# Kernel optimization log

Hardware: AMD Instinct MI355X
Metric: run time of the kernel (lower is better)

Reference implementation:

```python
import jax, jax.numpy as jnp
import numpy as np

BN_EPS = 1e-5

def bn(x, gamma, beta):
    # x: [N, C]; BatchNorm2d over (batch, spatial) == node axis here (training-mode batch stats)
    mu = x.mean(axis=0, keepdims=True)
    var = x.var(axis=0, keepdims=True)
    return (x - mu) * jax.lax.rsqrt(var + BN_EPS) * gamma + beta

def octree_conv(x, neigh, W):
    # x: [N, Cin]; neigh: [N, K] with values in [0, N], N == empty neighbor
    # W: [K, Cin, Cout]. Sparse octree conv = neighbor gather + contraction.
    xp = jnp.concatenate([x, jnp.zeros((1, x.shape[1]), x.dtype)], axis=0)  # zero row for empties
    g = xp[neigh]                                  # [N, K, Cin]
    return jnp.einsum('nkc,kcd->nd', g, W)         # [N, Cout]

def setup_inputs() -> dict:
    key = jax.random.key(0)
    ks = jax.random.split(key, 8)
    N, Cin, Cout, Cb, K = 60000, 256, 512, 128, 27
    s = 0.05
    return {
        'x': jax.random.normal(ks[0], (1, Cin, N, 1), jnp.float32),
        'neigh': jax.random.randint(ks[1], (N, K), 0, N + 1),
        'W1a': jax.random.normal(ks[2], (Cb, Cin), jnp.float32) * s,
        'g1a': jnp.ones((Cb,), jnp.float32), 'b1a': jnp.zeros((Cb,), jnp.float32),
        'W3': jax.random.normal(ks[3], (K, Cb, Cb), jnp.float32) * s,
        'g3': jnp.ones((Cb,), jnp.float32), 'b3': jnp.zeros((Cb,), jnp.float32),
        'W1b': jax.random.normal(ks[4], (Cout, Cb), jnp.float32) * s,
        'g1b': jnp.ones((Cout,), jnp.float32), 'b1b': jnp.zeros((Cout,), jnp.float32),
        'Wc': jax.random.normal(ks[5], (Cout, Cin), jnp.float32) * s,
        'gc': jnp.ones((Cout,), jnp.float32), 'bc': jnp.zeros((Cout,), jnp.float32),
    }

def reference(x, neigh, W1a, g1a, b1a, W3, g3, b3, W1b, g1b, b1b, Wc, gc, bc):
    h = jnp.squeeze(x, axis=(0, 3)).T                         # [N, Cin]
    c1 = jax.nn.relu(bn(h @ W1a.T, g1a, b1a))                 # 1x1 conv + BN + ReLU -> [N, Cb]
    c2 = jax.nn.relu(bn(octree_conv(c1, neigh, W3), g3, b3))  # sparse 3x3 octree conv + BN + ReLU
    c3 = bn(c2 @ W1b.T, g1b, b1b)                             # 1x1 conv + BN -> [N, Cout]
    sc = bn(h @ Wc.T, gc, bc)                                 # shortcut 1x1 conv + BN (Cin != Cout)
    out = jax.nn.relu(c3 + sc)
    return out.T[None, :, :, None]                            # [1, Cout, N, 1]
```

## Files before the change

kernel.cpp:

```cpp
#include <hip/hip_runtime.h>


typedef __bf16 bf16x8 __attribute__((ext_vector_type(8)));
typedef float f32x4 __attribute__((ext_vector_type(4)));
typedef unsigned short u16x8 __attribute__((ext_vector_type(8)));
typedef unsigned short u16x4 __attribute__((ext_vector_type(4)));

__device__ __forceinline__ unsigned short f2bfu(float f) {
  union { float f; unsigned u; } v; v.f = f;
  unsigned r = v.u + 0x7fffu + ((v.u >> 16) & 1u);
  return (unsigned short)(r >> 16);
}
__device__ __forceinline__ float bfu2f(unsigned short s) {
  union { unsigned u; float f; } v; v.u = ((unsigned)s) << 16;
  return v.f;
}

__device__ __forceinline__ void gload_lds16(const unsigned short* g, unsigned short* l) {
  __builtin_amdgcn_global_load_lds(
      (const __attribute__((address_space(1))) unsigned int*)(unsigned long long)g,
      (__attribute__((address_space(3))) unsigned int*)(unsigned int)(unsigned long long)l,
      16, 0, 0);
}

__device__ __forceinline__ int xcd_swz(int bid, int nwg) {
  int q = nwg >> 3, r = nwg & 7;
  int xcd = bid & 7, idx = bid >> 3;
  int base = xcd < r ? xcd * (q + 1) : r * (q + 1) + (xcd - r) * q;
  return base + idx;
}

__global__ __launch_bounds__(256) void prep_transpose(
    const float* __restrict__ x, unsigned short* __restrict__ h,
    const float* __restrict__ W1a, const float* __restrict__ W3,
    const float* __restrict__ W1b, const float* __restrict__ Wc,
    unsigned short* __restrict__ w1a, unsigned short* __restrict__ w3t,
    unsigned short* __restrict__ w1b, unsigned short* __restrict__ wc,
    int M, int MT) {
  __shared__ float tile[64][65];
  int t = threadIdx.x;
  if (blockIdx.x < 432) {
    int i = blockIdx.x * 256 + t;
    for (; i < 442368; i += 432 * 256) {
      if (i < 32768)  w1a[i] = f2bfu(W1a[i]);
      if (i < 65536)  w1b[i] = f2bfu(W1b[i]);
      if (i < 131072) wc[i]  = f2bfu(Wc[i]);
      int k = i >> 14, rr = i & 16383;
      int d = rr >> 7, c = rr & 127;
      w3t[i] = f2bfu(W3[(k << 14) + (c << 7) + d]);
    }
    return;
  }
  int bid = blockIdx.x - 432;
  int n0 = (bid % MT) * 64, c0 = (bid / MT) * 64;
  int nl = t & 63;
#pragma unroll
  for (int i = 0; i < 16; ++i) {
    int cl = i * 4 + (t >> 6);
    int n = n0 + nl;
    tile[cl][nl] = (n < M) ? x[(size_t)(c0 + cl) * M + n] : 0.f;
  }
  __syncthreads();
  int cl = t & 63;
#pragma unroll
  for (int i = 0; i < 16; ++i) {
    int nl2 = i * 4 + (t >> 6);
    int n = n0 + nl2;
    h[(size_t)n * 256 + c0 + cl] = f2bfu(tile[cl][nl2]);
  }
}

__global__ __launch_bounds__(512, 4) void gemm128(
    const unsigned short* __restrict__ A, const unsigned short* __restrict__ W,
    unsigned short* __restrict__ C, float* __restrict__ partials,
    int M, int Kd, int Nc, int ncol) {
  __shared__ unsigned short sA[2][128 * 64];
  __shared__ unsigned short sB[2][128 * 64];
  __shared__ float sStat[8][2][128];
  int t = threadIdx.x, wave = t >> 6, lane = t & 63;
  int flat = xcd_swz(blockIdx.x, gridDim.x);
  int n0 = (flat % ncol) * 128;
  int rowt = flat / ncol;
  int m0 = rowt * 128;
  int wr = wave >> 1, wcc = wave & 1;
  int l4 = lane >> 4, lc = lane & 15, lc7 = lc & 7;
  int lrow = lane >> 3, lch = lane & 7;
  f32x4 acc[2][4] = {};
  const int np = Kd >> 6;

  auto STAGE = [&](int p, int buf) {
    int k0 = p << 6;
#pragma unroll
    for (int i = 0; i < 2; ++i) {
      int row = wave * 16 + i * 8 + lrow;
      int sc = lch ^ (row & 7);
      gload_lds16(A + (size_t)(m0 + row) * Kd + k0 + sc * 8, &sA[buf][(wave * 16 + i * 8) * 64]);
    }
#pragma unroll
    for (int i = 0; i < 2; ++i) {
      int row = wave * 16 + i * 8 + lrow;
      int sc = lch ^ (row & 7);
      gload_lds16(W + (size_t)(n0 + row) * Kd + k0 + sc * 8, &sB[buf][(wave * 16 + i * 8) * 64]);
    }
  };
  auto COMPUTE = [&](int buf) {
#pragma unroll
    for (int kk = 0; kk < 2; ++kk) {
      bf16x8 af[2], bfr[4];
#pragma unroll
      for (int mi = 0; mi < 2; ++mi) {
        int row = wr * 32 + mi * 16 + lc;
        int chunk = (kk * 4 + l4) ^ lc7;
        af[mi] = __builtin_bit_cast(bf16x8, *(const u16x8*)(&sA[buf][row * 64 + chunk * 8]));
      }
#pragma unroll
      for (int ni = 0; ni < 4; ++ni) {
        int row = wcc * 64 + ni * 16 + lc;
        int chunk = (kk * 4 + l4) ^ lc7;
        bfr[ni] = __builtin_bit_cast(bf16x8, *(const u16x8*)(&sB[buf][row * 64 + chunk * 8]));
      }
      __builtin_amdgcn_s_setprio(1);
#pragma unroll
      for (int mi = 0; mi < 2; ++mi)
#pragma unroll
        for (int ni = 0; ni < 4; ++ni)
          acc[mi][ni] = __builtin_amdgcn_mfma_f32_16x16x32_bf16(af[mi], bfr[ni], acc[mi][ni], 0, 0, 0);
      __builtin_amdgcn_s_setprio(0);
    }
  };

  STAGE(0, 0);
  for (int p = 0; p < np; ++p) {
    int cur = p & 1;
    if (p < np - 1) {
      STAGE(p + 1, cur ^ 1);
      asm volatile("s_waitcnt vmcnt(4)" ::: "memory");
    } else {
      asm volatile("s_waitcnt vmcnt(0)" ::: "memory");
    }
    __builtin_amdgcn_sched_barrier(0);
    __builtin_amdgcn_s_barrier();
    __builtin_amdgcn_sched_barrier(0);
    COMPUTE(cur);
    __builtin_amdgcn_sched_barrier(0);
    __builtin_amdgcn_s_barrier();
  }

#pragma unroll
  for (int ni = 0; ni < 4; ++ni) {
    float s = 0.f, q = 0.f;
    int col = wcc * 64 + ni * 16 + lc;
#pragma unroll
    for (int mi = 0; mi < 2; ++mi)
#pragma unroll
      for (int j = 0; j < 4; ++j) {
        int n = m0 + wr * 32 + mi * 16 + l4 * 4 + j;
        unsigned short u = f2bfu(acc[mi][ni][j]);
        if (n < M) C[(size_t)n * Nc + n0 + col] = u;
        float v = bfu2f(u);
        s += v; q += v * v;
      }
    s += __shfl_xor(s, 16); s += __shfl_xor(s, 32);
    q += __shfl_xor(q, 16); q += __shfl_xor(q, 32);
    if (lane < 16) {
      sStat[wave][0][col] = s;
      sStat[wave][1][col] = q;
    }
  }
  __syncthreads();
  if (t < 128) {
    int wcs = t >> 6;
    float s = 0.f, q = 0.f;
#pragma unroll
    for (int g = 0; g < 4; ++g) {
      s += sStat[g * 2 + wcs][0][t];
      q += sStat[g * 2 + wcs][1][t];
    }
    partials[(size_t)rowt * (2 * Nc) + n0 + t] = s;
    partials[(size_t)rowt * (2 * Nc) + Nc + n0 + t] = q;
  }
}

__global__ __launch_bounds__(512, 4) void octree_sc(
    const unsigned short* __restrict__ c1, const int* __restrict__ neigh,
    const unsigned short* __restrict__ w3t, unsigned short* __restrict__ c2p,
    float* __restrict__ part12,
    const unsigned short* __restrict__ h, const unsigned short* __restrict__ wc,
    unsigned short* __restrict__ scp, float* __restrict__ partsc,
    int M, int MTO) {
  __shared__ unsigned short sA[2][128 * 64];
  __shared__ unsigned short sB[2][128 * 64];
  __shared__ union {
    unsigned short nidx[128 * 27];
    float stat[8][2][128];
  } u;
  int t = threadIdx.x, wave = t >> 6, lane = t & 63;
  int wr = wave >> 1, wcc = wave & 1;
  int l4 = lane >> 4, lc = lane & 15, lc7 = lc & 7;
  int lrow = lane >> 3, lch = lane & 7;
  f32x4 acc[2][4] = {};

  if (blockIdx.x < (unsigned)MTO) {
    int rowt = blockIdx.x;
    int m0 = rowt * 128;
    for (int i = t; i < 128 * 27; i += 512) {
      int row = i / 27;
      u.nidx[i] = (unsigned short)((m0 + row < M) ? neigh[(size_t)m0 * 27 + i] : M);
    }
    __syncthreads();

    auto STAGE = [&](int p, int buf) {
      int half = (p >= 27) ? 1 : 0;
      int k = p - half * 27;
      int c0 = half << 6;
#pragma unroll
      for (int i = 0; i < 2; ++i) {
        int row = wave * 16 + i * 8 + lrow;
        int nr = u.nidx[row * 27 + k];
        int sc = lch ^ (row & 7);
        gload_lds16(c1 + ((size_t)nr << 7) + c0 + sc * 8, &sA[buf][(wave * 16 + i * 8) * 64]);
      }
      const unsigned short* wk = w3t + ((size_t)k << 14);
#pragma unroll
      for (int i = 0; i < 2; ++i) {
        int row = wave * 16 + i * 8 + lrow;
        int sc = lch ^ (row & 7);
        gload_lds16(wk + ((size_t)row << 7) + c0 + sc * 8, &sB[buf][(wave * 16 + i * 8) * 64]);
      }
    };
    auto COMPUTE = [&](int buf) {
#pragma unroll
      for (int kk = 0; kk < 2; ++kk) {
        bf16x8 af[2], bfr[4];
#pragma unroll
        for (int mi = 0; mi < 2; ++mi) {
          int row = wr * 32 + mi * 16 + lc;
          int chunk = (kk * 4 + l4) ^ lc7;
          af[mi] = __builtin_bit_cast(bf16x8, *(const u16x8*)(&sA[buf][row * 64 + chunk * 8]));
        }
#pragma unroll
        for (int ni = 0; ni < 4; ++ni) {
          int row = wcc * 64 + ni * 16 + lc;
          int chunk = (kk * 4 + l4) ^ lc7;
          bfr[ni] = __builtin_bit_cast(bf16x8, *(const u16x8*)(&sB[buf][row * 64 + chunk * 8]));
        }
        __builtin_amdgcn_s_setprio(1);
#pragma unroll
        for (int mi = 0; mi < 2; ++mi)
#pragma unroll
          for (int ni = 0; ni < 4; ++ni)
            acc[mi][ni] = __builtin_amdgcn_mfma_f32_16x16x32_bf16(af[mi], bfr[ni], acc[mi][ni], 0, 0, 0);
        __builtin_amdgcn_s_setprio(0);
      }
    };

    STAGE(0, 0);
    for (int p = 0; p < 54; ++p) {
      int cur = p & 1;
      if (p < 53) {
        STAGE(p + 1, cur ^ 1);
        asm volatile("s_waitcnt vmcnt(4)" ::: "memory");
      } else {
        asm volatile("s_waitcnt vmcnt(0)" ::: "memory");
      }
      __builtin_amdgcn_sched_barrier(0);
      __builtin_amdgcn_s_barrier();
      __builtin_amdgcn_sched_barrier(0);
      COMPUTE(cur);
      __builtin_amdgcn_sched_barrier(0);
      __builtin_amdgcn_s_barrier();
    }

#pragma unroll
    for (int ni = 0; ni < 4; ++ni) {
      float s = 0.f, q = 0.f;
      int col = wcc * 64 + ni * 16 + lc;
#pragma unroll
      for (int mi = 0; mi < 2; ++mi)
#pragma unroll
        for (int j = 0; j < 4; ++j) {
          int n = m0 + wr * 32 + mi * 16 + l4 * 4 + j;
          unsigned short uo = f2bfu(acc[mi][ni][j]);
          if (n < M) c2p[(size_t)n * 128 + col] = uo;
          float v = bfu2f(uo);
          s += v; q += v * v;
        }
      s += __shfl_xor(s, 16); s += __shfl_xor(s, 32);
      q += __shfl_xor(q, 16); q += __shfl_xor(q, 32);
      if (lane < 16) {
        u.stat[wave][0][col] = s;
        u.stat[wave][1][col] = q;
      }
    }
    __syncthreads();
    if (t < 128) {
      int wcs = t >> 6;
      float s = 0.f, q = 0.f;
#pragma unroll
      for (int g = 0; g < 4; ++g) {
        s += u.stat[g * 2 + wcs][0][t];
        q += u.stat[g * 2 + wcs][1][t];
      }
      part12[(size_t)rowt * 256 + t] = s;
      part12[(size_t)rowt * 256 + 128 + t] = q;
    }
    return;
  }

  {
    int flat = xcd_swz(blockIdx.x - MTO, gridDim.x - MTO);
    int n0 = (flat & 3) * 128;
    int rowt = flat >> 2;
    int m0 = rowt * 128;

    auto STAGE = [&](int p, int buf) {
      int k0 = p << 6;
#pragma unroll
      for (int i = 0; i < 2; ++i) {
        int row = wave * 16 + i * 8 + lrow;
        int sc = lch ^ (row & 7);
        gload_lds16(h + (size_t)(m0 + row) * 256 + k0 + sc * 8, &sA[buf][(wave * 16 + i * 8) * 64]);
      }
#pragma unroll
      for (int i = 0; i < 2; ++i) {
        int row = wave * 16 + i * 8 + lrow;
        int sc = lch ^ (row & 7);
        gload_lds16(wc + (size_t)(n0 + row) * 256 + k0 + sc * 8, &sB[buf][(wave * 16 + i * 8) * 64]);
      }
    };
    auto COMPUTE = [&](int buf) {
#pragma unroll
      for (int kk = 0; kk < 2; ++kk) {
        bf16x8 af[2], bfr[4];
#pragma unroll
        for (int mi = 0; mi < 2; ++mi) {
          int row = wr * 32 + mi * 16 + lc;
          int chunk = (kk * 4 + l4) ^ lc7;
          af[mi] = __builtin_bit_cast(bf16x8, *(const u16x8*)(&sA[buf][row * 64 + chunk * 8]));
        }
#pragma unroll
        for (int ni = 0; ni < 4; ++ni) {
          int row = wcc * 64 + ni * 16 + lc;
          int chunk = (kk * 4 + l4) ^ lc7;
          bfr[ni] = __builtin_bit_cast(bf16x8, *(const u16x8*)(&sB[buf][row * 64 + chunk * 8]));
        }
        __builtin_amdgcn_s_setprio(1);
#pragma unroll
        for (int mi = 0; mi < 2; ++mi)
#pragma unroll
          for (int ni = 0; ni < 4; ++ni)
            acc[mi][ni] = __builtin_amdgcn_mfma_f32_16x16x32_bf16(af[mi], bfr[ni], acc[mi][ni], 0, 0, 0);
        __builtin_amdgcn_s_setprio(0);
      }
    };

    STAGE(0, 0);
    for (int p = 0; p < 4; ++p) {
      int cur = p & 1;
      if (p < 3) {
        STAGE(p + 1, cur ^ 1);
        asm volatile("s_waitcnt vmcnt(4)" ::: "memory");
      } else {
        asm volatile("s_waitcnt vmcnt(0)" ::: "memory");
      }
      __builtin_amdgcn_sched_barrier(0);
      __builtin_amdgcn_s_barrier();
      __builtin_amdgcn_sched_barrier(0);
      COMPUTE(cur);
      __builtin_amdgcn_sched_barrier(0);
      __builtin_amdgcn_s_barrier();
    }

#pragma unroll
    for (int ni = 0; ni < 4; ++ni) {
      float s = 0.f, q = 0.f;
      int col = wcc * 64 + ni * 16 + lc;
#pragma unroll
      for (int mi = 0; mi < 2; ++mi)
#pragma unroll
        for (int j = 0; j < 4; ++j) {
          int n = m0 + wr * 32 + mi * 16 + l4 * 4 + j;
          unsigned short uo = f2bfu(acc[mi][ni][j]);
          if (n < M) scp[(size_t)n * 512 + n0 + col] = uo;
          float v = bfu2f(uo);
          s += v; q += v * v;
        }
      s += __shfl_xor(s, 16); s += __shfl_xor(s, 32);
      q += __shfl_xor(q, 16); q += __shfl_xor(q, 32);
      if (lane < 16) {
        u.stat[wave][0][col] = s;
        u.stat[wave][1][col] = q;
      }
    }
    __syncthreads();
    if (t < 128) {
      int wcs = t >> 6;
      float s = 0.f, q = 0.f;
#pragma unroll
      for (int g = 0; g < 4; ++g) {
        s += u.stat[g * 2 + wcs][0][t];
        q += u.stat[g * 2 + wcs][1][t];
      }
      partsc[(size_t)rowt * 1024 + n0 + t] = s;
      partsc[(size_t)rowt * 1024 + 512 + n0 + t] = q;
    }
  }
}

__global__ __launch_bounds__(256) void bn_finalize(
    const float* __restrict__ partials, int nb, int C, int M,
    const float* __restrict__ g, const float* __restrict__ bt,
    float* __restrict__ ss) {
  int c = blockIdx.x;
  int t = threadIdx.x;
  float s = 0.f, s2 = 0.f;
  for (int b = t; b < nb; b += 256) {
    s += partials[(size_t)b * 2 * C + c];
    s2 += partials[(size_t)b * 2 * C + C + c];
  }
#pragma unroll
  for (int off = 32; off >= 1; off >>= 1) {
    s += __shfl_xor(s, off);
    s2 += __shfl_xor(s2, off);
  }
  __shared__ float sh[4][2];
  int wave = t >> 6, lane = t & 63;
  if (lane == 0) { sh[wave][0] = s; sh[wave][1] = s2; }
  __syncthreads();
  if (t == 0) {
    s = sh[0][0] + sh[1][0] + sh[2][0] + sh[3][0];
    s2 = sh[0][1] + sh[1][1] + sh[2][1] + sh[3][1];
    float mean = s / (float)M;
    float var = s2 / (float)M - mean * mean;
    float sc = g[c] * rsqrtf(var + 1e-5f);
    ss[c] = sc;
    ss[C + c] = bt[c] - mean * sc;
  }
}

__global__ __launch_bounds__(256) void bn_finalize_dual(
    const float* __restrict__ part12, const float* __restrict__ partsc,
    int nb, int M,
    const float* __restrict__ g3, const float* __restrict__ b3,
    const float* __restrict__ gc, const float* __restrict__ bc,
    float* __restrict__ ss2, float* __restrict__ sssc) {
  const float* partials; const float* g; const float* bt; float* ss;
  int c, C;
  if (blockIdx.x < 128) {
    partials = part12; g = g3; bt = b3; ss = ss2; c = blockIdx.x; C = 128;
  } else {
    partials = partsc; g = gc; bt = bc; ss = sssc; c = blockIdx.x - 128; C = 512;
  }
  int t = threadIdx.x;
  float s = 0.f, s2 = 0.f;
  for (int b = t; b < nb; b += 256) {
    s += partials[(size_t)b * 2 * C + c];
    s2 += partials[(size_t)b * 2 * C + C + c];
  }
#pragma unroll
  for (int off = 32; off >= 1; off >>= 1) {
    s += __shfl_xor(s, off);
    s2 += __shfl_xor(s2, off);
  }
  __shared__ float sh[4][2];
  int wave = t >> 6, lane = t & 63;
  if (lane == 0) { sh[wave][0] = s; sh[wave][1] = s2; }
  __syncthreads();
  if (t == 0) {
    s = sh[0][0] + sh[1][0] + sh[2][0] + sh[3][0];
    s2 = sh[0][1] + sh[1][1] + sh[2][1] + sh[3][1];
    float mean = s / (float)M;
    float var = s2 / (float)M - mean * mean;
    float sc = g[c] * rsqrtf(var + 1e-5f);
    ss[c] = sc;
    ss[C + c] = bt[c] - mean * sc;
  }
}

__global__ __launch_bounds__(256) void bnrelu(
    const unsigned short* __restrict__ P, const float* __restrict__ ss,
    unsigned short* __restrict__ Aout, int total, int total2, int Cmask) {
  int i = (blockIdx.x * 256 + threadIdx.x) * 8;
  if (i >= total2) return;
  u16x8 o = {0, 0, 0, 0, 0, 0, 0, 0};
  if (i < total) {
    u16x8 v = *(const u16x8*)(P + i);
    int c0 = i & Cmask;
    int C = Cmask + 1;
#pragma unroll
    for (int j = 0; j < 8; ++j) {
      float f = bfu2f(v[j]) * ss[c0 + j] + ss[C + c0 + j];
      o[j] = f2bfu(fmaxf(f, 0.f));
    }
  }
  *(u16x8*)(Aout + i) = o;
}

__global__ __launch_bounds__(256) void final_out(
    const unsigned short* __restrict__ c3p, const unsigned short* __restrict__ scp,
    const float* __restrict__ ss3, const float* __restrict__ sssc,
    float* __restrict__ out, int M) {
  __shared__ float tile[64][129];
  int n0 = blockIdx.x * 64, c0 = blockIdx.y * 128;
  int t = threadIdx.x;
  int rowg = t >> 5, cg = (t & 31) * 4;
#pragma unroll
  for (int ps = 0; ps < 8; ++ps) {
    int nl = ps * 8 + rowg;
    int n = n0 + nl;
    float v0 = 0.f, v1 = 0.f, v2 = 0.f, v3 = 0.f;
    if (n < M) {
      u16x4 a = *(const u16x4*)(c3p + (size_t)n * 512 + c0 + cg);
      u16x4 b = *(const u16x4*)(scp + (size_t)n * 512 + c0 + cg);
      int c = c0 + cg;
      v0 = fmaxf(bfu2f(a[0]) * ss3[c + 0] + ss3[512 + c + 0] + bfu2f(b[0]) * sssc[c + 0] + sssc[512 + c + 0], 0.f);
      v1 = fmaxf(bfu2f(a[1]) * ss3[c + 1] + ss3[512 + c + 1] + bfu2f(b[1]) * sssc[c + 1] + sssc[512 + c + 1], 0.f);
      v2 = fmaxf(bfu2f(a[2]) * ss3[c + 2] + ss3[512 + c + 2] + bfu2f(b[2]) * sssc[c + 2] + sssc[512 + c + 2], 0.f);
      v3 = fmaxf(bfu2f(a[3]) * ss3[c + 3] + ss3[512 + c + 3] + bfu2f(b[3]) * sssc[c + 3] + sssc[512 + c + 3], 0.f);
    }
    tile[nl][cg + 0] = v0;
    tile[nl][cg + 1] = v1;
    tile[nl][cg + 2] = v2;
    tile[nl][cg + 3] = v3;
  }
  __syncthreads();
  int nl = t & 63, cq = t >> 6;
  int n = n0 + nl;
  if (n < M) {
#pragma unroll
    for (int i = 0; i < 32; ++i) {
      int cl = i * 4 + cq;
      out[(size_t)(c0 + cl) * M + n] = tile[nl][cl];
    }
  }
}

extern "C" void kernel_launch(void* const* d_in, const int* in_sizes, int n_in,
                              void* d_out, int out_size, void* d_ws, size_t ws_size,
                              hipStream_t stream) {
  const float* x   = (const float*)d_in[0];
  const int* neigh = (const int*)d_in[1];
  const float* W1a = (const float*)d_in[2];
  const float* g1a = (const float*)d_in[3];
  const float* b1a = (const float*)d_in[4];
  const float* W3  = (const float*)d_in[5];
  const float* g3  = (const float*)d_in[6];
  const float* b3  = (const float*)d_in[7];
  const float* W1b = (const float*)d_in[8];
  const float* g1b = (const float*)d_in[9];
  const float* b1b = (const float*)d_in[10];
  const float* Wc  = (const float*)d_in[11];
  const float* gc  = (const float*)d_in[12];
  const float* bc  = (const float*)d_in[13];
  float* out = (float*)d_out;

  const int M = in_sizes[1] / 27;
  const int MT = (M + 63) / 64;
  const int MTO = (M + 127) / 128;

  char* ws = (char*)d_ws;
  unsigned short* h   = (unsigned short*)(ws + 0);
  unsigned short* wA  = (unsigned short*)(ws + 30736384);
  unsigned short* wP  = (unsigned short*)(ws + 46104576);
  unsigned short* c3p = (unsigned short*)(ws + 61464576);
  unsigned short* scp = (unsigned short*)(ws + 122904576);
  unsigned short* w1a = (unsigned short*)(ws + 184344576);
  unsigned short* w3t = (unsigned short*)(ws + 184410112);
  unsigned short* w1b = (unsigned short*)(ws + 185294848);
  unsigned short* wc  = (unsigned short*)(ws + 185425920);
  float* ss1  = (float*)(ws + 185688064);
  float* ss2  = (float*)(ws + 185692160);
  float* ss3  = (float*)(ws + 185696256);
  float* sssc = (float*)(ws + 185700352);

  float* part1  = (float*)(ws + 61464576);
  float* part12 = (float*)(ws + 61464576 + 1048576);
  float* partsc = (float*)(ws + 61464576 + 2097152);
  float* part3  = (float*)wP;

  prep_transpose<<<432 + MT * 4, 256, 0, stream>>>(
      x, h, W1a, W3, W1b, Wc, w1a, w3t, w1b, wc, M, MT);

  const int total = M * 128, total2 = (MT * 64) * 128;
  const int bnGrid = (total2 / 8 + 255) / 256;

  gemm128<<<MTO, 512, 0, stream>>>(h, w1a, wP, part1, M, 256, 128, 1);
  bn_finalize<<<128, 256, 0, stream>>>(part1, MTO, 128, M, g1a, b1a, ss1);
  bnrelu<<<bnGrid, 256, 0, stream>>>(wP, ss1, wA, total, total2, 127);

  octree_sc<<<MTO + 4 * MTO, 512, 0, stream>>>(
      wA, neigh, w3t, wP, part12, h, wc, scp, partsc, M, MTO);
  bn_finalize_dual<<<640, 256, 0, stream>>>(part12, partsc, MTO, M,
                                            g3, b3, gc, bc, ss2, sssc);
  bnrelu<<<bnGrid, 256, 0, stream>>>(wP, ss2, wA, total, total2, 127);

  gemm128<<<4 * MTO, 512, 0, stream>>>(wA, w1b, c3p, part3, M, 128, 512, 4);
  bn_finalize<<<512, 256, 0, stream>>>(part3, MTO, 512, M, g1b, b1b, ss3);

  final_out<<<dim3(MT, 4), 256, 0, stream>>>(c3p, scp, ss3, sssc, out, M);
}
```

Measured before the change: 222.6 us.

## Move shortcut GEMM from octree kernel into fused conv3/shortcut GEMM launch

The shortcut 1x1 GEMM (h·Wc) no longer shares a launch with the gather-heavy octree conv. It now runs alongside the final 1x1 GEMM (c2·W1b) in one kernel whose blocks are interleaved by role in groups of 8. The two matching BN finalizes are merged into a single 1024-block launch, and the partials buffer for the shortcut moves to a new workspace location. This balances similar-shaped dense GEMMs together and lets the octree kernel run alone, at the cost of the octree kernel no longer having independent work to overlap with its gather latency.

```diff
diff --git a/kernel.cpp b/kernel.cpp
--- a/kernel.cpp
+++ b/kernel.cpp
@@ -181,13 +181,10 @@
   }
 }
 
-__global__ __launch_bounds__(512, 4) void octree_sc(
+__global__ __launch_bounds__(512, 4) void octree_gemm(
     const unsigned short* __restrict__ c1, const int* __restrict__ neigh,
     const unsigned short* __restrict__ w3t, unsigned short* __restrict__ c2p,
-    float* __restrict__ part12,
-    const unsigned short* __restrict__ h, const unsigned short* __restrict__ wc,
-    unsigned short* __restrict__ scp, float* __restrict__ partsc,
-    int M, int MTO) {
+    float* __restrict__ part12, int M) {
   __shared__ unsigned short sA[2][128 * 64];
   __shared__ unsigned short sB[2][128 * 64];
   __shared__ union {
@@ -199,211 +196,230 @@
   int l4 = lane >> 4, lc = lane & 15, lc7 = lc & 7;
   int lrow = lane >> 3, lch = lane & 7;
   f32x4 acc[2][4] = {};
-
-  if (blockIdx.x < (unsigned)MTO) {
-    int rowt = blockIdx.x;
-    int m0 = rowt * 128;
-    for (int i = t; i < 128 * 27; i += 512) {
-      int row = i / 27;
-      u.nidx[i] = (unsigned short)((m0 + row < M) ? neigh[(size_t)m0 * 27 + i] : M);
-    }
-    __syncthreads();
-
-    auto STAGE = [&](int p, int buf) {
-      int half = (p >= 27) ? 1 : 0;
-      int k = p - half * 27;
-      int c0 = half << 6;
-#pragma unroll
-      for (int i = 0; i < 2; ++i) {
-        int row = wave * 16 + i * 8 + lrow;
-        int nr = u.nidx[row * 27 + k];
-        int sc = lch ^ (row & 7);
-        gload_lds16(c1 + ((size_t)nr << 7) + c0 + sc * 8, &sA[buf][(wave * 16 + i * 8) * 64]);
-      }
-      const unsigned short* wk = w3t + ((size_t)k << 14);
-#pragma unroll
-      for (int i = 0; i < 2; ++i) {
-        int row = wave * 16 + i * 8 + lrow;
-        int sc = lch ^ (row & 7);
-        gload_lds16(wk + ((size_t)row << 7) + c0 + sc * 8, &sB[buf][(wave * 16 + i * 8) * 64]);
-      }
-    };
-    auto COMPUTE = [&](int buf) {
-#pragma unroll
-      for (int kk = 0; kk < 2; ++kk) {
-        bf16x8 af[2], bfr[4];
-#pragma unroll
-        for (int mi = 0; mi < 2; ++mi) {
-          int row = wr * 32 + mi * 16 + lc;
-          int chunk = (kk * 4 + l4) ^ lc7;
-          af[mi] = __builtin_bit_cast(bf16x8, *(const u16x8*)(&sA[buf][row * 64 + chunk * 8]));
-        }
-#pragma unroll
-        for (int ni = 0; ni < 4; ++ni) {
-          int row = wcc * 64 + ni * 16 + lc;
-          int chunk = (kk * 4 + l4) ^ lc7;
-          bfr[ni] = __builtin_bit_cast(bf16x8, *(const u16x8*)(&sB[buf][row * 64 + chunk * 8]));
-        }
-        __builtin_amdgcn_s_setprio(1);
-#pragma unroll
-        for (int mi = 0; mi < 2; ++mi)
-#pragma unroll
-          for (int ni = 0; ni < 4; ++ni)
-            acc[mi][ni] = __builtin_amdgcn_mfma_f32_16x16x32_bf16(af[mi], bfr[ni], acc[mi][ni], 0, 0, 0);
-        __builtin_amdgcn_s_setprio(0);
-      }
-    };
-
-    STAGE(0, 0);
-    for (int p = 0; p < 54; ++p) {
-      int cur = p & 1;
-      if (p < 53) {
-        STAGE(p + 1, cur ^ 1);
-        asm volatile("s_waitcnt vmcnt(4)" ::: "memory");
-      } else {
-        asm volatile("s_waitcnt vmcnt(0)" ::: "memory");
-      }
-      __builtin_amdgcn_sched_barrier(0);
-      __builtin_amdgcn_s_barrier();
-      __builtin_amdgcn_sched_barrier(0);
-      COMPUTE(cur);
-      __builtin_amdgcn_sched_barrier(0);
-      __builtin_amdgcn_s_barrier();
-    }
-
-#pragma unroll
-    for (int ni = 0; ni < 4; ++ni) {
-      float s = 0.f, q = 0.f;
-      int col = wcc * 64 + ni * 16 + lc;
+  int rowt = blockIdx.x;
+  int m0 = rowt * 128;
+  for (int i = t; i < 128 * 27; i += 512) {
+    int row = i / 27;
+    u.nidx[i] = (unsigned short)((m0 + row < M) ? neigh[(size_t)m0 * 27 + i] : M);
+  }
+  __syncthreads();
+
+  auto STAGE = [&](int p, int buf) {
+    int half = (p >= 27) ? 1 : 0;
+    int k = p - half * 27;
+    int c0 = half << 6;
+#pragma unroll
+    for (int i = 0; i < 2; ++i) {
+      int row = wave * 16 + i * 8 + lrow;
+      int nr = u.nidx[row * 27 + k];
+      int sc = lch ^ (row & 7);
+      gload_lds16(c1 + ((size_t)nr << 7) + c0 + sc * 8, &sA[buf][(wave * 16 + i * 8) * 64]);
+    }
+    const unsigned short* wk = w3t + ((size_t)k << 14);
+#pragma unroll
+    for (int i = 0; i < 2; ++i) {
+      int row = wave * 16 + i * 8 + lrow;
+      int sc = lch ^ (row & 7);
+      gload_lds16(wk + ((size_t)row << 7) + c0 + sc * 8, &sB[buf][(wave * 16 + i * 8) * 64]);
+    }
+  };
+  auto COMPUTE = [&](int buf) {
+#pragma unroll
+    for (int kk = 0; kk < 2; ++kk) {
+      bf16x8 af[2], bfr[4];
+#pragma unroll
+      for (int mi = 0; mi < 2; ++mi) {
+        int row = wr * 32 + mi * 16 + lc;
+        int chunk = (kk * 4 + l4) ^ lc7;
+        af[mi] = __builtin_bit_cast(bf16x8, *(const u16x8*)(&sA[buf][row * 64 + chunk * 8]));
+      }
+#pragma unroll
+      for (int ni = 0; ni < 4; ++ni) {
+        int row = wcc * 64 + ni * 16 + lc;
+        int chunk = (kk * 4 + l4) ^ lc7;
+        bfr[ni] = __builtin_bit_cast(bf16x8, *(const u16x8*)(&sB[buf][row * 64 + chunk * 8]));
+      }
+      __builtin_amdgcn_s_setprio(1);
 #pragma unroll
       for (int mi = 0; mi < 2; ++mi)
 #pragma unroll
-        for (int j = 0; j < 4; ++j) {
-          int n = m0 + wr * 32 + mi * 16 + l4 * 4 + j;
-          unsigned short uo = f2bfu(acc[mi][ni][j]);
-          if (n < M) c2p[(size_t)n * 128 + col] = uo;
-          float v = bfu2f(uo);
-          s += v; q += v * v;
-        }
-      s += __shfl_xor(s, 16); s += __shfl_xor(s, 32);
-      q += __shfl_xor(q, 16); q += __shfl_xor(q, 32);
-      if (lane < 16) {
-        u.stat[wave][0][col] = s;
-        u.stat[wave][1][col] = q;
-      }
-    }
-    __syncthreads();
-    if (t < 128) {
-      int wcs = t >> 6;
-      float s = 0.f, q = 0.f;
-#pragma unroll
-      for (int g = 0; g < 4; ++g) {
-        s += u.stat[g * 2 + wcs][0][t];
-        q += u.stat[g * 2 + wcs][1][t];
-      }
-      part12[(size_t)rowt * 256 + t] = s;
-      part12[(size_t)rowt * 256 + 128 + t] = q;
-    }
-    return;
-  }
-
-  {
-    int flat = xcd_swz(blockIdx.x - MTO, gridDim.x - MTO);
-    int n0 = (flat & 3) * 128;
-    int rowt = flat >> 2;
-    int m0 = rowt * 128;
-
-    auto STAGE = [&](int p, int buf) {
-      int k0 = p << 6;
-#pragma unroll
-      for (int i = 0; i < 2; ++i) {
-        int row = wave * 16 + i * 8 + lrow;
-        int sc = lch ^ (row & 7);
-        gload_lds16(h + (size_t)(m0 + row) * 256 + k0 + sc * 8, &sA[buf][(wave * 16 + i * 8) * 64]);
-      }
-#pragma unroll
-      for (int i = 0; i < 2; ++i) {
-        int row = wave * 16 + i * 8 + lrow;
-        int sc = lch ^ (row & 7);
-        gload_lds16(wc + (size_t)(n0 + row) * 256 + k0 + sc * 8, &sB[buf][(wave * 16 + i * 8) * 64]);
-      }
-    };
-    auto COMPUTE = [&](int buf) {
-#pragma unroll
-      for (int kk = 0; kk < 2; ++kk) {
-        bf16x8 af[2], bfr[4];
-#pragma unroll
-        for (int mi = 0; mi < 2; ++mi) {
-          int row = wr * 32 + mi * 16 + lc;
-          int chunk = (kk * 4 + l4) ^ lc7;
-          af[mi] = __builtin_bit_cast(bf16x8, *(const u16x8*)(&sA[buf][row * 64 + chunk * 8]));
-        }
-#pragma unroll
-        for (int ni = 0; ni < 4; ++ni) {
-          int row = wcc * 64 + ni * 16 + lc;
-          int chunk = (kk * 4 + l4) ^ lc7;
-          bfr[ni] = __builtin_bit_cast(bf16x8, *(const u16x8*)(&sB[buf][row * 64 + chunk * 8]));
-        }
-        __builtin_amdgcn_s_setprio(1);
-#pragma unroll
-        for (int mi = 0; mi < 2; ++mi)
-#pragma unroll
-          for (int ni = 0; ni < 4; ++ni)
-            acc[mi][ni] = __builtin_amdgcn_mfma_f32_16x16x32_bf16(af[mi], bfr[ni], acc[mi][ni], 0, 0, 0);
-        __builtin_amdgcn_s_setprio(0);
-      }
-    };
-
-    STAGE(0, 0);
-    for (int p = 0; p < 4; ++p) {
-      int cur = p & 1;
-      if (p < 3) {
-        STAGE(p + 1, cur ^ 1);
-        asm volatile("s_waitcnt vmcnt(4)" ::: "memory");
-      } else {
-        asm volatile("s_waitcnt vmcnt(0)" ::: "memory");
-      }
-      __builtin_amdgcn_sched_barrier(0);
-      __builtin_amdgcn_s_barrier();
-      __builtin_amdgcn_sched_barrier(0);
-      COMPUTE(cur);
-      __builtin_amdgcn_sched_barrier(0);
-      __builtin_amdgcn_s_barrier();
-    }
-
-#pragma unroll
-    for (int ni = 0; ni < 4; ++ni) {
-      float s = 0.f, q = 0.f;
-      int col = wcc * 64 + ni * 16 + lc;
+        for (int ni = 0; ni < 4; ++ni)
+          acc[mi][ni] = __builtin_amdgcn_mfma_f32_16x16x32_bf16(af[mi], bfr[ni], acc[mi][ni], 0, 0, 0);
+      __builtin_amdgcn_s_setprio(0);
+    }
+  };
+
+  STAGE(0, 0);
+  for (int p = 0; p < 54; ++p) {
+    int cur = p & 1;
+    if (p < 53) {
+      STAGE(p + 1, cur ^ 1);
+      asm volatile("s_waitcnt vmcnt(4)" ::: "memory");
+    } else {
+      asm volatile("s_waitcnt vmcnt(0)" ::: "memory");
+    }
+    __builtin_amdgcn_sched_barrier(0);
+    __builtin_amdgcn_s_barrier();
+    __builtin_amdgcn_sched_barrier(0);
+    COMPUTE(cur);
+    __builtin_amdgcn_sched_barrier(0);
+    __builtin_amdgcn_s_barrier();
+  }
+
+#pragma unroll
+  for (int ni = 0; ni < 4; ++ni) {
+    float s = 0.f, q = 0.f;
+    int col = wcc * 64 + ni * 16 + lc;
+#pragma unroll
+    for (int mi = 0; mi < 2; ++mi)
+#pragma unroll
+      for (int j = 0; j < 4; ++j) {
+        int n = m0 + wr * 32 + mi * 16 + l4 * 4 + j;
+        unsigned short uo = f2bfu(acc[mi][ni][j]);
+        if (n < M) c2p[(size_t)n * 128 + col] = uo;
+        float v = bfu2f(uo);
+        s += v; q += v * v;
+      }
+    s += __shfl_xor(s, 16); s += __shfl_xor(s, 32);
+    q += __shfl_xor(q, 16); q += __shfl_xor(q, 32);
+    if (lane < 16) {
+      u.stat[wave][0][col] = s;
+      u.stat[wave][1][col] = q;
+    }
+  }
+  __syncthreads();
+  if (t < 128) {
+    int wcs = t >> 6;
+    float s = 0.f, q = 0.f;
+#pragma unroll
+    for (int g = 0; g < 4; ++g) {
+      s += u.stat[g * 2 + wcs][0][t];
+      q += u.stat[g * 2 + wcs][1][t];
+    }
+    part12[(size_t)rowt * 256 + t] = s;
+    part12[(size_t)rowt * 256 + 128 + t] = q;
+  }
+}
+
+__global__ __launch_bounds__(512, 4) void gemm3_sc(
+    const unsigned short* __restrict__ wA, const unsigned short* __restrict__ w1b,
+    unsigned short* __restrict__ c3p, float* __restrict__ part3,
+    const unsigned short* __restrict__ h, const unsigned short* __restrict__ wc,
+    unsigned short* __restrict__ scp, float* __restrict__ partsc,
+    int M, int MTO) {
+  __shared__ unsigned short sA[2][128 * 64];
+  __shared__ unsigned short sB[2][128 * 64];
+  __shared__ float sStat[8][2][128];
+  int t = threadIdx.x, wave = t >> 6, lane = t & 63;
+  int bid = blockIdx.x;
+  int role = (bid >> 3) & 1;
+  int sub = ((bid >> 4) << 3) | (bid & 7);
+  const int nsub = 4 * MTO;
+  int flat = xcd_swz(sub, ((nsub + 7) >> 3) << 3);
+  if (flat >= nsub) return;
+  const unsigned short* A; const unsigned short* W;
+  unsigned short* C; float* partials; int Kd;
+  if (role == 0) { A = wA; W = w1b; C = c3p; partials = part3; Kd = 128; }
+  else           { A = h;  W = wc;  C = scp; partials = partsc; Kd = 256; }
+  int n0 = (flat & 3) * 128;
+  int rowt = flat >> 2;
+  int m0 = rowt * 128;
+  int wr = wave >> 1, wcc = wave & 1;
+  int l4 = lane >> 4, lc = lane & 15, lc7 = lc & 7;
+  int lrow = lane >> 3, lch = lane & 7;
+  f32x4 acc[2][4] = {};
+  const int np = Kd >> 6;
+
+  auto STAGE = [&](int p, int buf) {
+    int k0 = p << 6;
+#pragma unroll
+    for (int i = 0; i < 2; ++i) {
+      int row = wave * 16 + i * 8 + lrow;
+      int sc = lch ^ (row & 7);
+      gload_lds16(A + (size_t)(m0 + row) * Kd + k0 + sc * 8, &sA[buf][(wave * 16 + i * 8) * 64]);
+    }
+#pragma unroll
+    for (int i = 0; i < 2; ++i) {
+      int row = wave * 16 + i * 8 + lrow;
+      int sc = lch ^ (row & 7);
+      gload_lds16(W + (size_t)(n0 + row) * Kd + k0 + sc * 8, &sB[buf][(wave * 16 + i * 8) * 64]);
+    }
+  };
+  auto COMPUTE = [&](int buf) {
+#pragma unroll
+    for (int kk = 0; kk < 2; ++kk) {
+      bf16x8 af[2], bfr[4];
+#pragma unroll
+      for (int mi = 0; mi < 2; ++mi) {
+        int row = wr * 32 + mi * 16 + lc;
+        int chunk = (kk * 4 + l4) ^ lc7;
+        af[mi] = __builtin_bit_cast(bf16x8, *(const u16x8*)(&sA[buf][row * 64 + chunk * 8]));
+      }
+#pragma unroll
+      for (int ni = 0; ni < 4; ++ni) {
+        int row = wcc * 64 + ni * 16 + lc;
+        int chunk = (kk * 4 + l4) ^ lc7;
+        bfr[ni] = __builtin_bit_cast(bf16x8, *(const u16x8*)(&sB[buf][row * 64 + chunk * 8]));
+      }
+      __builtin_amdgcn_s_setprio(1);
 #pragma unroll
       for (int mi = 0; mi < 2; ++mi)
 #pragma unroll
-        for (int j = 0; j < 4; ++j) {
-          int n = m0 + wr * 32 + mi * 16 + l4 * 4 + j;
-          unsigned short uo = f2bfu(acc[mi][ni][j]);
-          if (n < M) scp[(size_t)n * 512 + n0 + col] = uo;
-          float v = bfu2f(uo);
-          s += v; q += v * v;
-        }
-      s += __shfl_xor(s, 16); s += __shfl_xor(s, 32);
-      q += __shfl_xor(q, 16); q += __shfl_xor(q, 32);
-      if (lane < 16) {
-        u.stat[wave][0][col] = s;
-        u.stat[wave][1][col] = q;
-      }
-    }
-    __syncthreads();
-    if (t < 128) {
-      int wcs = t >> 6;
-      float s = 0.f, q = 0.f;
-#pragma unroll
-      for (int g = 0; g < 4; ++g) {
-        s += u.stat[g * 2 + wcs][0][t];
-        q += u.stat[g * 2 + wcs][1][t];
-      }
-      partsc[(size_t)rowt * 1024 + n0 + t] = s;
-      partsc[(size_t)rowt * 1024 + 512 + n0 + t] = q;
-    }
+        for (int ni = 0; ni < 4; ++ni)
+          acc[mi][ni] = __builtin_amdgcn_mfma_f32_16x16x32_bf16(af[mi], bfr[ni], acc[mi][ni], 0, 0, 0);
+      __builtin_amdgcn_s_setprio(0);
+    }
+  };
+
+  STAGE(0, 0);
+  for (int p = 0; p < np; ++p) {
+    int cur = p & 1;
+    if (p < np - 1) {
+      STAGE(p + 1, cur ^ 1);
+      asm volatile("s_waitcnt vmcnt(4)" ::: "memory");
+    } else {
+      asm volatile("s_waitcnt vmcnt(0)" ::: "memory");
+    }
+    __builtin_amdgcn_sched_barrier(0);
+    __builtin_amdgcn_s_barrier();
+    __builtin_amdgcn_sched_barrier(0);
+    COMPUTE(cur);
+    __builtin_amdgcn_sched_barrier(0);
+    __builtin_amdgcn_s_barrier();
+  }
+
+#pragma unroll
+  for (int ni = 0; ni < 4; ++ni) {
+    float s = 0.f, q = 0.f;
+    int col = wcc * 64 + ni * 16 + lc;
+#pragma unroll
+    for (int mi = 0; mi < 2; ++mi)
+#pragma unroll
+      for (int j = 0; j < 4; ++j) {
+        int n = m0 + wr * 32 + mi * 16 + l4 * 4 + j;
+        unsigned short uo = f2bfu(acc[mi][ni][j]);
+        if (n < M) C[(size_t)n * 512 + n0 + col] = uo;
+        float v = bfu2f(uo);
+        s += v; q += v * v;
+      }
+    s += __shfl_xor(s, 16); s += __shfl_xor(s, 32);
+    q += __shfl_xor(q, 16); q += __shfl_xor(q, 32);
+    if (lane < 16) {
+      sStat[wave][0][col] = s;
+      sStat[wave][1][col] = q;
+    }
+  }
+  __syncthreads();
+  if (t < 128) {
+    int wcs = t >> 6;
+    float s = 0.f, q = 0.f;
+#pragma unroll
+    for (int g = 0; g < 4; ++g) {
+      s += sStat[g * 2 + wcs][0][t];
+      q += sStat[g * 2 + wcs][1][t];
+    }
+    partials[(size_t)rowt * 1024 + n0 + t] = s;
+    partials[(size_t)rowt * 1024 + 512 + n0 + t] = q;
   }
 }
 
@@ -438,24 +454,21 @@
   }
 }
 
-__global__ __launch_bounds__(256) void bn_finalize_dual(
-    const float* __restrict__ part12, const float* __restrict__ partsc,
+__global__ __launch_bounds__(256) void bn_finalize_dual512(
+    const float* __restrict__ part3, const float* __restrict__ partsc,
     int nb, int M,
-    const float* __restrict__ g3, const float* __restrict__ b3,
+    const float* __restrict__ g1b, const float* __restrict__ b1b,
     const float* __restrict__ gc, const float* __restrict__ bc,
-    float* __restrict__ ss2, float* __restrict__ sssc) {
+    float* __restrict__ ss3, float* __restrict__ sssc) {
   const float* partials; const float* g; const float* bt; float* ss;
-  int c, C;
-  if (blockIdx.x < 128) {
-    partials = part12; g = g3; bt = b3; ss = ss2; c = blockIdx.x; C = 128;
-  } else {
-    partials = partsc; g = gc; bt = bc; ss = sssc; c = blockIdx.x - 128; C = 512;
-  }
+  int c;
+  if (blockIdx.x < 512) { partials = part3; g = g1b; bt = b1b; ss = ss3; c = blockIdx.x; }
+  else { partials = partsc; g = gc; bt = bc; ss = sssc; c = blockIdx.x - 512; }
   int t = threadIdx.x;
   float s = 0.f, s2 = 0.f;
   for (int b = t; b < nb; b += 256) {
-    s += partials[(size_t)b * 2 * C + c];
-    s2 += partials[(size_t)b * 2 * C + C + c];
+    s += partials[(size_t)b * 1024 + c];
+    s2 += partials[(size_t)b * 1024 + 512 + c];
   }
 #pragma unroll
   for (int off = 32; off >= 1; off >>= 1) {
@@ -473,7 +486,7 @@
     float var = s2 / (float)M - mean * mean;
     float sc = g[c] * rsqrtf(var + 1e-5f);
     ss[c] = sc;
-    ss[C + c] = bt[c] - mean * sc;
+    ss[512 + c] = bt[c] - mean * sc;
   }
 }
 
@@ -575,8 +588,8 @@
 
   float* part1  = (float*)(ws + 61464576);
   float* part12 = (float*)(ws + 61464576 + 1048576);
-  float* partsc = (float*)(ws + 61464576 + 2097152);
   float* part3  = (float*)wP;
+  float* partsc = (float*)(ws + 46104576 + 4194304);
 
   prep_transpose<<<432 + MT * 4, 256, 0, stream>>>(
       x, h, W1a, W3, W1b, Wc, w1a, w3t, w1b, wc, M, MT);
@@ -588,14 +601,14 @@
   bn_finalize<<<128, 256, 0, stream>>>(part1, MTO, 128, M, g1a, b1a, ss1);
   bnrelu<<<bnGrid, 256, 0, stream>>>(wP, ss1, wA, total, total2, 127);
 
-  octree_sc<<<MTO + 4 * MTO, 512, 0, stream>>>(
-      wA, neigh, w3t, wP, part12, h, wc, scp, partsc, M, MTO);
-  bn_finalize_dual<<<640, 256, 0, stream>>>(part12, partsc, MTO, M,
-                                            g3, b3, gc, bc, ss2, sssc);
+  octree_gemm<<<MTO, 512, 0, stream>>>(wA, neigh, w3t, wP, part12, M);
+  bn_finalize<<<128, 256, 0, stream>>>(part12, MTO, 128, M, g3, b3, ss2);
   bnrelu<<<bnGrid, 256, 0, stream>>>(wP, ss2, wA, total, total2, 127);
 
-  gemm128<<<4 * MTO, 512, 0, stream>>>(wA, w1b, c3p, part3, M, 128, 512, 4);
-  bn_finalize<<<512, 256, 0, stream>>>(part3, MTO, 512, M, g1b, b1b, ss3);
+  gemm3_sc<<<2 * ((4 * MTO + 7) / 8) * 8, 512, 0, stream>>>(
+      wA, w1b, c3p, part3, h, wc, scp, partsc, M, MTO);
+  bn_finalize_dual512<<<1024, 256, 0, stream>>>(part3, partsc, MTO, M,
+                                                g1b, b1b, gc, bc, ss3, sssc);
 
   final_out<<<dim3(MT, 4), 256, 0, stream>>>(c3p, scp, ss3, sssc, out, M);
 }
```

Measured after the change: 226.3 us. No clear change (+1.7%).
